# Kernel optimization log

Measured on AMD Instinct MI355X. Metric: run time of the kernel, lower is better.

## Reference

```python
import jax, jax.numpy as jnp
import numpy as np

N = 30000
IN_DIM = 256
OUT_DIM = 256
H = 4
HEAD_DIM = OUT_DIM // H  # 64
NUM_EDGE_TYPES = 20
NUM_USED_TYPES = 5  # len(EDGE_TYPES); global indices 0..4
E_PER_TYPE = 40000


def setup_inputs() -> dict:
    key = jax.random.key(0)
    ks = jax.random.split(key, 12)
    s = 0.05
    return {
        "h": jax.random.normal(ks[0], (N, IN_DIM), jnp.float32),
        "edge_src": jax.random.randint(ks[1], (NUM_USED_TYPES, E_PER_TYPE), 0, N, jnp.int64 if jax.config.jax_enable_x64 else jnp.int32),
        "edge_tgt": jax.random.randint(ks[2], (NUM_USED_TYPES, E_PER_TYPE), 0, N, jnp.int64 if jax.config.jax_enable_x64 else jnp.int32),
        "kqv_weight": jax.random.normal(ks[3], (3 * OUT_DIM, IN_DIM), jnp.float32) * s,
        "kqv_bias": jax.random.normal(ks[4], (3 * OUT_DIM,), jnp.float32) * s,
        "out_weight": jax.random.normal(ks[5], (OUT_DIM, OUT_DIM), jnp.float32) * s,
        "out_bias": jax.random.normal(ks[6], (OUT_DIM,), jnp.float32) * s,
        "k_rel": jax.random.normal(ks[7], (NUM_EDGE_TYPES, HEAD_DIM, HEAD_DIM), jnp.float32) * s,
        "v_rel": jax.random.normal(ks[8], (NUM_EDGE_TYPES, HEAD_DIM, HEAD_DIM), jnp.float32) * s,
        "skip": jax.random.normal(ks[9], (1,), jnp.float32),
        "p_rel": jax.random.normal(ks[10], (NUM_USED_TYPES, H), jnp.float32),
    }


def reference(h, edge_src, edge_tgt, kqv_weight, kqv_bias, out_weight, out_bias,
              k_rel, v_rel, skip, p_rel):
    n = h.shape[0]
    T, E = edge_src.shape
    d = HEAD_DIM

    # fused KQV projection: [N, 3*D]
    kqv = h @ kqv_weight.T + kqv_bias
    K, Q, V = jnp.split(kqv, 3, axis=-1)
    K = K.reshape(n, H, d)
    Q = Q.reshape(n, H, d)
    V = V.reshape(n, H, d)

    et = jnp.arange(T)  # global edge-type indices 0..T-1
    k_r = k_rel[et]     # [T, d, d]
    v_r = v_rel[et]

    # gather per-edge, per-type; apply relation matmuls
    K_rel = jnp.einsum('tehd,tdf->tehf', K[edge_src], k_r)  # [T,E,H,d]
    V_rel = jnp.einsum('tehd,tdf->tehf', V[edge_src], v_r)
    Q_tgt = Q[edge_tgt]                                     # [T,E,H,d]

    scale = float(d) ** (-0.5)
    alpha = (Q_tgt * K_rel).sum(-1) * scale                 # [T,E,H]
    alpha = alpha * p_rel[et][:, None, :]                   # multiplicative prior

    # flatten all edge types
    TE = T * E
    alpha = alpha.reshape(TE, H)
    V_rel = V_rel.reshape(TE, H, d)
    tgt_all = edge_tgt.reshape(TE)

    # segmented softmax over incoming edges per target node
    amax = jax.ops.segment_max(alpha, tgt_all, num_segments=n)       # [N,H]
    exp_alpha = jnp.exp(alpha - amax[tgt_all])
    exp_sum = jax.ops.segment_sum(exp_alpha, tgt_all, num_segments=n)
    attn = exp_alpha / (exp_sum[tgt_all] + 1e-16)                    # [TE,H]

    msg = attn[..., None] * V_rel                                    # [TE,H,d]
    out = jax.ops.segment_sum(msg, tgt_all, num_segments=n)          # [N,H,d]
    out = out.reshape(n, OUT_DIM)

    out = jax.nn.gelu(out, approximate=False)
    out = out @ out_weight.T + out_bias

    a = jax.nn.sigmoid(skip)  # [1], broadcasts
    return a * out + (1.0 - a) * h
```

## Files before the change

### kernel.cpp

```cpp
#include <hip/hip_runtime.h>
#include <hip/hip_bf16.h>
#include <math.h>

#define N_NODES 30000
#define NHEAD   4
#define HDIM    64
#define NTYPES  5
#define EPT     40000
#define TE      (NTYPES * EPT)
#define KDIM    256
#define NCAT    1792
#define NBLK    118

typedef __attribute__((ext_vector_type(8))) short short8;
typedef __attribute__((ext_vector_type(4))) float f32x4;

__device__ __forceinline__ unsigned short f2bf(float f) {
    __hip_bfloat16 h = __float2bfloat16(f);
    return *reinterpret_cast<unsigned short*>(&h);
}
__device__ __forceinline__ float bf2f(unsigned short u) {
    return __uint_as_float((unsigned)u << 16);
}

__device__ __forceinline__ void gload16(const unsigned short* g, unsigned short* l) {
    __builtin_amdgcn_global_load_lds((const __attribute__((address_space(1))) void*)g,
                                     (__attribute__((address_space(3))) void*)l, 16, 0, 0);
}

__global__ __launch_bounds__(256) void init_kernel(int* __restrict__ deg) {
    const int gid = blockIdx.x * blockDim.x + threadIdx.x;
    if (gid < N_NODES) deg[gid] = 0;
}

__global__ __launch_bounds__(256) void hist_kernel(const int* __restrict__ etgt,
                                                   int* __restrict__ deg) {
    const int stride = gridDim.x * blockDim.x;
    for (int i = blockIdx.x * blockDim.x + threadIdx.x; i < TE; i += stride)
        atomicAdd(&deg[etgt[i]], 1);
}

__global__ __launch_bounds__(256) void scan1_kernel(const int* __restrict__ deg,
                                                    int* __restrict__ bsum) {
    __shared__ int ws[4];
    const int t = threadIdx.x;
    const int gid = blockIdx.x * 256 + t;
    int d = (gid < N_NODES) ? deg[gid] : 0;
    d += __shfl_xor(d, 1);
    d += __shfl_xor(d, 2);
    d += __shfl_xor(d, 4);
    d += __shfl_xor(d, 8);
    d += __shfl_xor(d, 16);
    d += __shfl_xor(d, 32);
    if ((t & 63) == 0) ws[t >> 6] = d;
    __syncthreads();
    if (t == 0) bsum[blockIdx.x] = ws[0] + ws[1] + ws[2] + ws[3];
}

__global__ __launch_bounds__(128) void scan2_kernel(const int* __restrict__ bsum,
                                                    int* __restrict__ boff) {
    __shared__ int s[128];
    const int t = threadIdx.x;
    s[t] = (t < NBLK) ? bsum[t] : 0;
    __syncthreads();
    for (int d = 1; d < 128; d <<= 1) {
        const int v = (t >= d) ? s[t - d] : 0;
        __syncthreads();
        s[t] += v;
        __syncthreads();
    }
    if (t < NBLK) boff[t] = (t > 0) ? s[t - 1] : 0;
}

__global__ __launch_bounds__(256) void scan3_kernel(const int* __restrict__ deg,
                                                    const int* __restrict__ boff,
                                                    int* __restrict__ off,
                                                    int* __restrict__ cursor) {
    __shared__ int s[256];
    const int t = threadIdx.x;
    const int gid = blockIdx.x * 256 + t;
    const int d = (gid < N_NODES) ? deg[gid] : 0;
    s[t] = d;
    __syncthreads();
    for (int dd = 1; dd < 256; dd <<= 1) {
        const int v = (t >= dd) ? s[t - dd] : 0;
        __syncthreads();
        s[t] += v;
        __syncthreads();
    }
    if (gid < N_NODES) {
        const int excl = s[t] - d + boff[blockIdx.x];
        off[gid] = excl;
        cursor[gid] = excl;
    }
}

__global__ __launch_bounds__(256) void scatter_kernel(const int* __restrict__ etgt,
                                                      const int* __restrict__ esrc,
                                                      int* __restrict__ cursor,
                                                      int* __restrict__ perm) {
    const int stride = gridDim.x * blockDim.x;
    for (int e = blockIdx.x * blockDim.x + threadIdx.x; e < TE; e += stride) {
        const int pos = atomicAdd(&cursor[etgt[e]], 1);
        perm[pos] = esrc[e] | ((e / EPT) << 16);
    }
}

__global__ __launch_bounds__(256) void prep_all(const float* __restrict__ kqv_w,
                                                const float* __restrict__ kqv_b,
                                                const float* __restrict__ k_rel,
                                                const float* __restrict__ p_rel,
                                                const float* __restrict__ h,
                                                const float* __restrict__ v_rel,
                                                const float* __restrict__ out_w,
                                                unsigned short* __restrict__ Wcat,
                                                float* __restrict__ bias_cat,
                                                unsigned short* __restrict__ hb,
                                                unsigned short* __restrict__ vrelT,
                                                unsigned short* __restrict__ Wob) {
    const int bid = blockIdx.x;
    const int tid = threadIdx.x;
    if (bid < 1792) {
        const int r = bid, f = tid;
        if (r < 1280) {
            const int t = r >> 8, hh = (r >> 6) & 3, d = r & 63;
            const float sc = 0.125f * p_rel[t * NHEAD + hh];
            float acc = 0.f;
#pragma unroll
            for (int fp = 0; fp < 64; ++fp)
                acc = fmaf(kqv_w[(size_t)(hh * 64 + fp) * 256 + f], k_rel[t * 4096 + fp * 64 + d], acc);
            Wcat[(size_t)r * 256 + f] = f2bf(acc * sc);
            if (f == 0) {
                float b = 0.f;
#pragma unroll
                for (int fp = 0; fp < 64; ++fp)
                    b = fmaf(kqv_b[hh * 64 + fp], k_rel[t * 4096 + fp * 64 + d], b);
                bias_cat[r] = b * sc;
            }
        } else {
            const int src_row = r - 1024;
            Wcat[(size_t)r * 256 + f] = f2bf(kqv_w[(size_t)src_row * 256 + f]);
            if (f == 0) bias_cat[r] = kqv_b[src_row];
        }
    } else if (bid < 9292) {
        const int i = (bid - 1792) * 256 + tid;
        const float4 v = ((const float4*)h)[i];
        ushort4 u;
        u.x = f2bf(v.x); u.y = f2bf(v.y); u.z = f2bf(v.z); u.w = f2bf(v.w);
        ((ushort4*)hb)[i] = u;
    } else if (bid < 9372) {
        const int idx = (bid - 9292) * 256 + tid;
        if (idx < 64 * 320) {
            const int f = idx / 320, k = idx - f * 320;
            vrelT[f * 320 + k] = f2bf(v_rel[(k >> 6) * 4096 + (k & 63) * 64 + f]);
        }
    } else {
        const int i = (bid - 9372) * 256 + tid;
        Wob[i] = f2bf(out_w[i]);
    }
}

__global__ __launch_bounds__(256) void mfma_gemm(const unsigned short* __restrict__ hb,
                                                 const unsigned short* __restrict__ Wcat,
                                                 const float* __restrict__ bias_cat,
                                                 unsigned short* __restrict__ Ccat) {
    __shared__ unsigned short As[2][128 * 32];
    __shared__ unsigned short Bs[2][128 * 32];
    const int orig = blockIdx.x;
    const int xcd = orig & 7, pos = orig >> 3;
    const int q = 3290 / 8, r = 3290 % 8;
    const int wgid = (xcd < r ? xcd * (q + 1) : r * (q + 1) + (xcd - r) * q) + pos;
    const int brow0 = (wgid / 14) * 128;
    const int bcol0 = (wgid % 14) * 128;

    const int t = threadIdx.x;
    const int wid = t >> 6, lane = t & 63;
    const int wr = wid >> 1, wc = wid & 1;
    const int lrow = lane & 15, kb = lane >> 4;
    const int srow = lane >> 2;
    const int schunk = ((lane & 3) ^ ((lane >> 3) & 3)) * 8;
    const int rchunk = (kb ^ ((lrow >> 1) & 3)) * 8;

    const int arow0 = min(brow0 + wid * 16 + srow, N_NODES - 1);
    const int arow1 = min(brow0 + 64 + wid * 16 + srow, N_NODES - 1);
    const int brw0 = bcol0 + wid * 16 + srow;
    const int brw1 = bcol0 + 64 + wid * 16 + srow;

    auto stage = [&](int buf, int kt) {
        gload16(hb + (size_t)arow0 * KDIM + kt + schunk, &As[buf][wid * 512]);
        gload16(hb + (size_t)arow1 * KDIM + kt + schunk, &As[buf][2048 + wid * 512]);
        gload16(Wcat + (size_t)brw0 * KDIM + kt + schunk, &Bs[buf][wid * 512]);
        gload16(Wcat + (size_t)brw1 * KDIM + kt + schunk, &Bs[buf][2048 + wid * 512]);
    };

    f32x4 acc[4][4];
#pragma unroll
    for (int m = 0; m < 4; ++m)
#pragma unroll
        for (int n = 0; n < 4; ++n) acc[m][n] = (f32x4)0.f;

    stage(0, 0);
    __syncthreads();
    int cur = 0;
    for (int kt = 0; kt < KDIM; kt += 32) {
        if (kt + 32 < KDIM) stage(cur ^ 1, kt + 32);
        short8 af[4], bfr[4];
#pragma unroll
        for (int m = 0; m < 4; ++m)
            af[m] = *(const short8*)&As[cur][(wr * 64 + m * 16 + lrow) * 32 + rchunk];
#pragma unroll
        for (int n = 0; n < 4; ++n)
            bfr[n] = *(const short8*)&Bs[cur][(wc * 64 + n * 16 + lrow) * 32 + rchunk];
#pragma unroll
        for (int m = 0; m < 4; ++m)
#pragma unroll
            for (int n = 0; n < 4; ++n)
                acc[m][n] = __builtin_amdgcn_mfma_f32_16x16x32_bf16(af[m], bfr[n], acc[m][n], 0, 0, 0);
        __syncthreads();
        cur ^= 1;
    }

    unsigned short* Ts = &As[0][0];
    float bias4[4];
#pragma unroll
    for (int n = 0; n < 4; ++n) bias4[n] = bias_cat[bcol0 + wc * 64 + n * 16 + lrow];
    const int lrw = wr * 16 + kb * 4;
    const int lcw = wc * 64 + lrow;
#pragma unroll
    for (int m = 0; m < 4; ++m) {
        __syncthreads();
#pragma unroll
        for (int n = 0; n < 4; ++n)
#pragma unroll
            for (int v = 0; v < 4; ++v)
                Ts[(lrw + v) * 132 + lcw + n * 16] = f2bf(acc[m][n][v] + bias4[n]);
        __syncthreads();
#pragma unroll
        for (int rd = 0; rd < 2; ++rd) {
            const int lr = (t >> 4) + rd * 16;
            const int c0 = (t & 15) * 8;
            const int grow = brow0 + (lr >> 4) * 64 + m * 16 + (lr & 15);
            if (grow < N_NODES) {
                const uint2 lo = *(const uint2*)&Ts[lr * 132 + c0];
                const uint2 hi = *(const uint2*)&Ts[lr * 132 + c0 + 4];
                const uint4 o = make_uint4(lo.x, lo.y, hi.x, hi.y);
                *(uint4*)&Ccat[(size_t)grow * NCAT + bcol0 + c0] = o;
            }
        }
    }
}

__global__ __launch_bounds__(256) void edge_fused(const unsigned short* __restrict__ Ccat,
                                                  const int* __restrict__ off,
                                                  const int* __restrict__ perm,
                                                  unsigned short* __restrict__ Acat) {
    const int wid = threadIdx.x >> 6, lane = threadIdx.x & 63;
    const int tgt = (blockIdx.x << 2) + wid;
    const int h = lane >> 4, f0 = (lane & 15) << 2;
    const int off0 = off[tgt];
    const int off1 = (tgt == N_NODES - 1) ? TE : off[tgt + 1];
    const ushort4 qu = *(const ushort4*)(Ccat + (size_t)tgt * NCAT + 1280 + (h << 6) + f0);
    const float qx = bf2f(qu.x), qy = bf2f(qu.y), qz = bf2f(qu.z), qw = bf2f(qu.w);
    const int voff = 1536 + (h << 6) + f0;
    float es = 0.f;
    float4 a0 = make_float4(0, 0, 0, 0), a1 = a0, a2 = a0, a3 = a0, a4 = a0;
    int i = off0;
    while (i < off1) {
        const bool two = (i + 1 < off1);
        const int pk0 = perm[i];
        const int pk1 = two ? perm[i + 1] : pk0;
        const int s0 = pk0 & 0xFFFF, t0 = pk0 >> 16;
        const int s1 = pk1 & 0xFFFF, t1 = pk1 >> 16;
        const size_t rb0 = (size_t)s0 * NCAT, rb1 = (size_t)s1 * NCAT;
        const ushort4 ku0 = *(const ushort4*)(Ccat + rb0 + ((t0 * 4 + h) << 6) + f0);
        const ushort4 vu0 = *(const ushort4*)(Ccat + rb0 + voff);
        const ushort4 ku1 = *(const ushort4*)(Ccat + rb1 + ((t1 * 4 + h) << 6) + f0);
        const ushort4 vu1 = *(const ushort4*)(Ccat + rb1 + voff);
        float p0 = qx * bf2f(ku0.x) + qy * bf2f(ku0.y) + qz * bf2f(ku0.z) + qw * bf2f(ku0.w);
        float p1 = qx * bf2f(ku1.x) + qy * bf2f(ku1.y) + qz * bf2f(ku1.z) + qw * bf2f(ku1.w);
        p0 += __shfl_xor(p0, 1); p1 += __shfl_xor(p1, 1);
        p0 += __shfl_xor(p0, 2); p1 += __shfl_xor(p1, 2);
        p0 += __shfl_xor(p0, 4); p1 += __shfl_xor(p1, 4);
        p0 += __shfl_xor(p0, 8); p1 += __shfl_xor(p1, 8);
        {
            const float ex = __expf(p0);
            es += ex;
            const float mx = ex * bf2f(vu0.x), my = ex * bf2f(vu0.y);
            const float mz = ex * bf2f(vu0.z), mw = ex * bf2f(vu0.w);
            if (t0 == 0)      { a0.x += mx; a0.y += my; a0.z += mz; a0.w += mw; }
            else if (t0 == 1) { a1.x += mx; a1.y += my; a1.z += mz; a1.w += mw; }
            else if (t0 == 2) { a2.x += mx; a2.y += my; a2.z += mz; a2.w += mw; }
            else if (t0 == 3) { a3.x += mx; a3.y += my; a3.z += mz; a3.w += mw; }
            else              { a4.x += mx; a4.y += my; a4.z += mz; a4.w += mw; }
        }
        if (two) {
            const float ex = __expf(p1);
            es += ex;
            const float mx = ex * bf2f(vu1.x), my = ex * bf2f(vu1.y);
            const float mz = ex * bf2f(vu1.z), mw = ex * bf2f(vu1.w);
            if (t1 == 0)      { a0.x += mx; a0.y += my; a0.z += mz; a0.w += mw; }
            else if (t1 == 1) { a1.x += mx; a1.y += my; a1.z += mz; a1.w += mw; }
            else if (t1 == 2) { a2.x += mx; a2.y += my; a2.z += mz; a2.w += mw; }
            else if (t1 == 3) { a3.x += mx; a3.y += my; a3.z += mz; a3.w += mw; }
            else              { a4.x += mx; a4.y += my; a4.z += mz; a4.w += mw; }
        }
        i += two ? 2 : 1;
    }
    const float inv = 1.f / (es + 1e-16f);
    const size_t rr = (size_t)tgt * NHEAD + h;
    unsigned short* base = Acat + rr * (NTYPES * HDIM) + f0;
    ushort4 u;
    u.x = f2bf(a0.x * inv); u.y = f2bf(a0.y * inv); u.z = f2bf(a0.z * inv); u.w = f2bf(a0.w * inv);
    *(ushort4*)(base + 0 * HDIM) = u;
    u.x = f2bf(a1.x * inv); u.y = f2bf(a1.y * inv); u.z = f2bf(a1.z * inv); u.w = f2bf(a1.w * inv);
    *(ushort4*)(base + 1 * HDIM) = u;
    u.x = f2bf(a2.x * inv); u.y = f2bf(a2.y * inv); u.z = f2bf(a2.z * inv); u.w = f2bf(a2.w * inv);
    *(ushort4*)(base + 2 * HDIM) = u;
    u.x = f2bf(a3.x * inv); u.y = f2bf(a3.y * inv); u.z = f2bf(a3.z * inv); u.w = f2bf(a3.w * inv);
    *(ushort4*)(base + 3 * HDIM) = u;
    u.x = f2bf(a4.x * inv); u.y = f2bf(a4.y * inv); u.z = f2bf(a4.z * inv); u.w = f2bf(a4.w * inv);
    *(ushort4*)(base + 4 * HDIM) = u;
}

__global__ __launch_bounds__(256) void tail_fused(const unsigned short* __restrict__ Acat,
                                                  const unsigned short* __restrict__ vrelT,
                                                  const unsigned short* __restrict__ Wob,
                                                  const float* __restrict__ bias,
                                                  float* __restrict__ C,
                                                  const unsigned short* __restrict__ hres,
                                                  const float* __restrict__ skip) {
    __shared__ unsigned short Gs[64 * 264];
    const int t = threadIdx.x;
    const int wid = t >> 6, lane = t & 63;
    const int lrow = lane & 15, kb = lane >> 4;
    const int n0 = blockIdx.x * 64;
    const size_t ar0 = (size_t)n0 * 4;

    {
        f32x4 acc[4][4];
#pragma unroll
        for (int m = 0; m < 4; ++m)
#pragma unroll
            for (int n = 0; n < 4; ++n) acc[m][n] = (f32x4)0.f;

        size_t arow[4];
#pragma unroll
        for (int m = 0; m < 4; ++m)
            arow[m] = min(ar0 + (size_t)(wid * 64 + m * 16 + lrow), (size_t)120000 - 1);

        for (int kt = 0; kt < 320; kt += 32) {
            short8 af[4], bf_[4];
#pragma unroll
            for (int m = 0; m < 4; ++m)
                af[m] = *(const short8*)(Acat + arow[m] * 320 + kt + kb * 8);
#pragma unroll
            for (int n = 0; n < 4; ++n)
                bf_[n] = *(const short8*)(vrelT + (size_t)(n * 16 + lrow) * 320 + kt + kb * 8);
#pragma unroll
            for (int m = 0; m < 4; ++m)
#pragma unroll
                for (int n = 0; n < 4; ++n)
                    acc[m][n] = __builtin_amdgcn_mfma_f32_16x16x32_bf16(af[m], bf_[n], acc[m][n], 0, 0, 0);
        }
#pragma unroll
        for (int m = 0; m < 4; ++m)
#pragma unroll
            for (int v = 0; v < 4; ++v) {
                const int lr = wid * 64 + m * 16 + kb * 4 + v;
#pragma unroll
                for (int n = 0; n < 4; ++n) {
                    const int col = n * 16 + lrow;
                    const float x = acc[m][n][v];
                    const float g = 0.5f * x * (1.f + erff(x * 0.7071067811865475f));
                    Gs[(lr >> 2) * 264 + (lr & 3) * 64 + col] = f2bf(g);
                }
            }
    }
    __syncthreads();

    {
        const int wc = wid;
        f32x4 acc[4][4];
#pragma unroll
        for (int m = 0; m < 4; ++m)
#pragma unroll
            for (int n = 0; n < 4; ++n) acc[m][n] = (f32x4)0.f;

        for (int kt = 0; kt < 256; kt += 32) {
            short8 af[4], bfr[4];
#pragma unroll
            for (int m = 0; m < 4; ++m)
                af[m] = *(const short8*)&Gs[(m * 16 + lrow) * 264 + kt + kb * 8];
#pragma unroll
            for (int n = 0; n < 4; ++n)
                bfr[n] = *(const short8*)(Wob + (size_t)(wc * 64 + n * 16 + lrow) * 256 + kt + kb * 8);
#pragma unroll
            for (int m = 0; m < 4; ++m)
#pragma unroll
                for (int n = 0; n < 4; ++n)
                    acc[m][n] = __builtin_amdgcn_mfma_f32_16x16x32_bf16(af[m], bfr[n], acc[m][n], 0, 0, 0);
        }

        const float s = skip[0];
        const float sa = 1.f / (1.f + expf(-s));
        const float sb = 1.f - sa;
        float bias4[4];
#pragma unroll
        for (int n = 0; n < 4; ++n) bias4[n] = bias[wc * 64 + n * 16 + lrow];
#pragma unroll
        for (int m = 0; m < 4; ++m) {
            const int gr0 = n0 + m * 16 + kb * 4;
#pragma unroll
            for (int v = 0; v < 4; ++v) {
                const int grow = gr0 + v;
                if (grow < N_NODES) {
#pragma unroll
                    for (int n = 0; n < 4; ++n) {
                        const int gcol = wc * 64 + n * 16 + lrow;
                        const float val = acc[m][n][v] + bias4[n];
                        C[(size_t)grow * 256 + gcol] = sa * val + sb * bf2f(hres[(size_t)grow * 256 + gcol]);
                    }
                }
            }
        }
    }
}

extern "C" void kernel_launch(void* const* d_in, const int* in_sizes, int n_in,
                              void* d_out, int out_size, void* d_ws, size_t ws_size,
                              hipStream_t stream) {
    const float* h      = (const float*)d_in[0];
    const int*   esrc   = (const int*)d_in[1];
    const int*   etgt   = (const int*)d_in[2];
    const float* kqv_w  = (const float*)d_in[3];
    const float* kqv_b  = (const float*)d_in[4];
    const float* out_w  = (const float*)d_in[5];
    const float* out_b  = (const float*)d_in[6];
    const float* k_rel  = (const float*)d_in[7];
    const float* v_rel  = (const float*)d_in[8];
    const float* skip   = (const float*)d_in[9];
    const float* p_rel  = (const float*)d_in[10];
    float* out = (float*)d_out;

    float* ws = (float*)d_ws;
    unsigned short* Ccat     = (unsigned short*)ws;
    int*            deg      = (int*)(ws + 26880000);
    int*            off      = (int*)(ws + 26910000);
    int*            cursor   = (int*)(ws + 26940000);
    int*            perm     = (int*)(ws + 26970000);
    unsigned short* Acat     = (unsigned short*)(ws + 31010000);
    unsigned short* vrelT    = (unsigned short*)(ws + 50210000);
    unsigned short* Wob      = (unsigned short*)(ws + 50220240);
    unsigned short* hb       = (unsigned short*)(ws + 50253008);
    int*            bsum     = (int*)(ws + 54093008);
    int*            boff     = (int*)(ws + 54093126);
    unsigned short* Wcat     = (unsigned short*)(ws + 45370000);
    float*          bias_cat = ws + 45600000;

    hipLaunchKernelGGL(init_kernel, dim3(NBLK), dim3(256), 0, stream, deg);
    hipLaunchKernelGGL(hist_kernel, dim3(782), dim3(256), 0, stream, etgt, deg);
    hipLaunchKernelGGL(scan1_kernel, dim3(NBLK), dim3(256), 0, stream, deg, bsum);
    hipLaunchKernelGGL(scan2_kernel, dim3(1), dim3(128), 0, stream, bsum, boff);
    hipLaunchKernelGGL(scan3_kernel, dim3(NBLK), dim3(256), 0, stream, deg, boff, off, cursor);
    hipLaunchKernelGGL(scatter_kernel, dim3(782), dim3(256), 0, stream, etgt, esrc, cursor, perm);
    hipLaunchKernelGGL(prep_all, dim3(9628), dim3(256), 0, stream,
                       kqv_w, kqv_b, k_rel, p_rel, h, v_rel, out_w,
                       Wcat, bias_cat, hb, vrelT, Wob);
    hipLaunchKernelGGL(mfma_gemm, dim3(3290), dim3(256), 0, stream,
                       hb, Wcat, bias_cat, Ccat);
    hipLaunchKernelGGL(edge_fused, dim3(N_NODES / 4), dim3(256), 0, stream,
                       Ccat, off, perm, Acat);
    hipLaunchKernelGGL(tail_fused, dim3(469), dim3(256), 0, stream,
                       Acat, vrelT, Wob, out_b, out, hb, skip);
}
```

Measured before the change: 178.1 us.

## Load GEMM MFMA operands directly from global memory instead of LDS staging

The KQV projection GEMM drops its double-buffered LDS staging (global_load_lds with swizzled chunks) and has each lane load its bf16 A and B fragments straight from global memory into registers. This removes the LDS traffic and per-iteration barriers and shrinks shared memory to only the epilogue transpose buffer. The cost is redundant global/L2 reads across waves that share rows or columns, and no software prefetch overlapping loads with MFMA.

```diff
diff --git a/kernel.cpp b/kernel.cpp
--- a/kernel.cpp
+++ b/kernel.cpp
@@ -21,11 +21,6 @@
 }
 __device__ __forceinline__ float bf2f(unsigned short u) {
     return __uint_as_float((unsigned)u << 16);
-}
-
-__device__ __forceinline__ void gload16(const unsigned short* g, unsigned short* l) {
-    __builtin_amdgcn_global_load_lds((const __attribute__((address_space(1))) void*)g,
-                                     (__attribute__((address_space(3))) void*)l, 16, 0, 0);
 }
 
 __global__ __launch_bounds__(256) void init_kernel(int* __restrict__ deg) {
@@ -164,8 +159,7 @@
                                                  const unsigned short* __restrict__ Wcat,
                                                  const float* __restrict__ bias_cat,
                                                  unsigned short* __restrict__ Ccat) {
-    __shared__ unsigned short As[2][128 * 32];
-    __shared__ unsigned short Bs[2][128 * 32];
+    __shared__ unsigned short Ts[32 * 132];
     const int orig = blockIdx.x;
     const int xcd = orig & 7, pos = orig >> 3;
     const int q = 3290 / 8, r = 3290 % 8;
@@ -177,21 +171,15 @@
     const int wid = t >> 6, lane = t & 63;
     const int wr = wid >> 1, wc = wid & 1;
     const int lrow = lane & 15, kb = lane >> 4;
-    const int srow = lane >> 2;
-    const int schunk = ((lane & 3) ^ ((lane >> 3) & 3)) * 8;
-    const int rchunk = (kb ^ ((lrow >> 1) & 3)) * 8;
-
-    const int arow0 = min(brow0 + wid * 16 + srow, N_NODES - 1);
-    const int arow1 = min(brow0 + 64 + wid * 16 + srow, N_NODES - 1);
-    const int brw0 = bcol0 + wid * 16 + srow;
-    const int brw1 = bcol0 + 64 + wid * 16 + srow;
-
-    auto stage = [&](int buf, int kt) {
-        gload16(hb + (size_t)arow0 * KDIM + kt + schunk, &As[buf][wid * 512]);
-        gload16(hb + (size_t)arow1 * KDIM + kt + schunk, &As[buf][2048 + wid * 512]);
-        gload16(Wcat + (size_t)brw0 * KDIM + kt + schunk, &Bs[buf][wid * 512]);
-        gload16(Wcat + (size_t)brw1 * KDIM + kt + schunk, &Bs[buf][2048 + wid * 512]);
-    };
+
+    size_t arow[4];
+#pragma unroll
+    for (int m = 0; m < 4; ++m)
+        arow[m] = (size_t)min(brow0 + wr * 64 + m * 16 + lrow, N_NODES - 1);
+    size_t brow_[4];
+#pragma unroll
+    for (int n = 0; n < 4; ++n)
+        brow_[n] = (size_t)(bcol0 + wc * 64 + n * 16 + lrow);
 
     f32x4 acc[4][4];
 #pragma unroll
@@ -199,28 +187,21 @@
 #pragma unroll
         for (int n = 0; n < 4; ++n) acc[m][n] = (f32x4)0.f;
 
-    stage(0, 0);
-    __syncthreads();
-    int cur = 0;
     for (int kt = 0; kt < KDIM; kt += 32) {
-        if (kt + 32 < KDIM) stage(cur ^ 1, kt + 32);
         short8 af[4], bfr[4];
 #pragma unroll
         for (int m = 0; m < 4; ++m)
-            af[m] = *(const short8*)&As[cur][(wr * 64 + m * 16 + lrow) * 32 + rchunk];
+            af[m] = *(const short8*)(hb + arow[m] * KDIM + kt + kb * 8);
 #pragma unroll
         for (int n = 0; n < 4; ++n)
-            bfr[n] = *(const short8*)&Bs[cur][(wc * 64 + n * 16 + lrow) * 32 + rchunk];
+            bfr[n] = *(const short8*)(Wcat + brow_[n] * KDIM + kt + kb * 8);
 #pragma unroll
         for (int m = 0; m < 4; ++m)
 #pragma unroll
             for (int n = 0; n < 4; ++n)
                 acc[m][n] = __builtin_amdgcn_mfma_f32_16x16x32_bf16(af[m], bfr[n], acc[m][n], 0, 0, 0);
-        __syncthreads();
-        cur ^= 1;
-    }
-
-    unsigned short* Ts = &As[0][0];
+    }
+
     float bias4[4];
 #pragma unroll
     for (int n = 0; n < 4; ++n) bias4[n] = bias_cat[bcol0 + wc * 64 + n * 16 + lrow];
```

New measurement: 233.8 us. 1.31x slower.
